# Kernel tuning notes

Hardware: AMD Instinct MI355X
Metric: run time of the kernel (lower is better)

## Reference

```python
import jax, jax.numpy as jnp
import numpy as np

N = 20000      # total atoms per branch
M = 12         # max neighbors
ORIG = 92      # orig_atom_fea_len
NBR = 41       # nbr_fea_len
F = 64         # atom_fea_len
H = 128        # h_fea_len
NCONV = 3
NH = 1
NCRYS = 400    # crystals in batch
EPS = 1e-5


def _bn_params(k, c):
    k1, k2, k3, k4 = jax.random.split(k, 4)
    g = 1.0 + 0.1 * jax.random.normal(k1, (c,), jnp.float32)
    b = 0.1 * jax.random.normal(k2, (c,), jnp.float32)
    m = 0.1 * jax.random.normal(k3, (c,), jnp.float32)
    v = 1.0 + 0.1 * jnp.abs(jax.random.normal(k4, (c,), jnp.float32))
    return jnp.stack([g, b, m, v], axis=0)  # (4, c)


def setup_inputs():
    key = jax.random.key(0)
    ks = iter(jax.random.split(key, 64))
    inp = {}
    for s in ('A', 'B'):
        inp[f'atom_fea_{s}'] = jax.random.normal(next(ks), (N, ORIG), jnp.float32)
        inp[f'nbr_fea_{s}'] = jax.random.uniform(next(ks), (N, M, NBR), jnp.float32)
        inp[f'nbr_fea_idx_{s}'] = jax.random.randint(next(ks), (N, M), 0, N)
        inp[f'crystal_atom_idx_{s}'] = jnp.sort(jax.random.randint(next(ks), (N,), 0, NCRYS))
        inp[f'emb_W_{s}'] = 0.05 * jax.random.normal(next(ks), (ORIG, F), jnp.float32)
        inp[f'emb_b_{s}'] = jnp.zeros((F,), jnp.float32)
        inp[f'conv_W_{s}'] = 0.05 * jax.random.normal(next(ks), (NCONV, 2 * F + NBR, 2 * F), jnp.float32)
        inp[f'conv_b_{s}'] = jnp.zeros((NCONV, 2 * F), jnp.float32)
        inp[f'conv_bn1_{s}'] = jnp.stack([_bn_params(next(ks), 2 * F) for _ in range(NCONV)])  # (NCONV,4,2F)
        inp[f'conv_bn2_{s}'] = jnp.stack([_bn_params(next(ks), F) for _ in range(NCONV)])      # (NCONV,4,F)
        inp[f'dense_W_{s}'] = 0.05 * jax.random.normal(next(ks), (F, H), jnp.float32)
        inp[f'dense_b_{s}'] = jnp.zeros((H,), jnp.float32)
    inp['ff_W'] = 0.05 * jax.random.normal(next(ks), (NH, H, H), jnp.float32)
    inp['ff_b'] = jnp.zeros((NH, H), jnp.float32)
    inp['out_W'] = 0.05 * jax.random.normal(next(ks), (H, 1), jnp.float32)
    inp['out_b'] = jnp.zeros((1,), jnp.float32)
    return inp


def _bn_eval(x, p):
    # eval-mode batchnorm: (x - mean) / sqrt(var + eps) * gamma + beta
    g, b, m, v = p[0], p[1], p[2], p[3]
    return (x - m) * (g * jax.lax.rsqrt(v + EPS)) + b


def _conv_layer(x, nbr_fea, nbr_idx, W, b, bn1, bn2):
    # x: (N,F); nbr_fea: (N,M,NBR); nbr_idx: (N,M)
    nbr = x[nbr_idx]                                              # gather (N,M,F)
    self_f = jnp.broadcast_to(x[:, None, :], nbr.shape)          # (N,M,F)
    tot = jnp.concatenate([self_f, nbr, nbr_fea], axis=2)        # (N,M,2F+NBR)
    z = _bn_eval(tot @ W + b, bn1)                               # (N,M,2F)
    filt, core = jnp.split(z, 2, axis=2)
    s = jnp.sum(jax.nn.sigmoid(filt) * jax.nn.softplus(core), axis=1)  # (N,F)
    s = _bn_eval(s, bn2)
    return jax.nn.softplus(x + s)


def _pool_mean(x, seg):
    s = jax.ops.segment_sum(x, seg, num_segments=NCRYS)
    cnt = jax.ops.segment_sum(jnp.ones((x.shape[0], 1), x.dtype), seg, num_segments=NCRYS)
    return s / jnp.maximum(cnt, 1.0)


def _branch(atom_fea, nbr_fea, nbr_idx, seg, emb_W, emb_b, conv_W, conv_b, bn1, bn2, dense_W, dense_b):
    a = atom_fea @ emb_W + emb_b
    for i in range(NCONV):
        a = _conv_layer(a, nbr_fea, nbr_idx, conv_W[i], conv_b[i], bn1[i], bn2[i])
    return jax.nn.softplus(_pool_mean(a, seg) @ dense_W + dense_b)  # (NCRYS,H)


def reference(atom_fea_A, nbr_fea_A, nbr_fea_idx_A, crystal_atom_idx_A,
              atom_fea_B, nbr_fea_B, nbr_fea_idx_B, crystal_atom_idx_B,
              emb_W_A, emb_b_A, conv_W_A, conv_b_A, conv_bn1_A, conv_bn2_A, dense_W_A, dense_b_A,
              emb_W_B, emb_b_B, conv_W_B, conv_b_B, conv_bn1_B, conv_bn2_B, dense_W_B, dense_b_B,
              ff_W, ff_b, out_W, out_b):
    crys_A = _branch(atom_fea_A, nbr_fea_A, nbr_fea_idx_A, crystal_atom_idx_A,
                     emb_W_A, emb_b_A, conv_W_A, conv_b_A, conv_bn1_A, conv_bn2_A, dense_W_A, dense_b_A)
    crys_B = _branch(atom_fea_B, nbr_fea_B, nbr_fea_idx_B, crystal_atom_idx_B,
                     emb_W_B, emb_b_B, conv_W_B, conv_b_B, conv_bn1_B, conv_bn2_B, dense_W_B, dense_b_B)
    crys = jnp.abs(crys_A - crys_B)  # combine_features == 'subtract_abs'
    for i in range(NH):              # dropout is identity in eval mode
        crys = jax.nn.softplus(crys @ ff_W[i] + ff_b[i])
    return crys @ out_W + out_b      # (NCRYS, 1)
```

## Files before the change

kernel.cpp:

```cpp
#include <hip/hip_runtime.h>


constexpr int NATOM = 20000;
constexpr int MNBR  = 12;
constexpr int ORIG  = 92;
constexpr int NBRF  = 41;
constexpr int F     = 64;
constexpr int H     = 128;
constexpr int NCONV = 3;
constexpr int NCRYS = 400;

#define DEVFN __device__ __forceinline__

typedef __attribute__((ext_vector_type(8))) short short8;
typedef __attribute__((ext_vector_type(4))) float f32x4;

DEVFN float softplusf(float x) {
    return fmaxf(x, 0.f) + __logf(1.f + __expf(-fabsf(x)));
}
DEVFN float sigmoidf(float x) {
    return __builtin_amdgcn_rcpf(1.f + __expf(-x));
}
DEVFN unsigned short f2bf(float x) {
    union { float f; unsigned u; } v{x};
    unsigned r = v.u + 0x7FFF + ((v.u >> 16) & 1);
    return (unsigned short)(r >> 16);
}
DEVFN float bf2f(unsigned short h) {
    union { unsigned u; float f; } v;
    v.u = (unsigned)h << 16;
    return v.f;
}
DEVFN unsigned pk2(float a, float b) {
    return (unsigned)f2bf(a) | ((unsigned)f2bf(b) << 16);
}
DEVFN unsigned short f2h(float x) {
    _Float16 h = (_Float16)x;
    union { _Float16 h; unsigned short u; } v{h};
    return v.u;
}
DEVFN float h2f(unsigned short u) {
    union { unsigned short u; _Float16 h; } v{u};
    return (float)v.h;
}
DEVFN unsigned packlo(unsigned a, unsigned b) { return (a & 0xffffu) | (b << 16); }
DEVFN unsigned packhi(unsigned a, unsigned b) { return (a >> 16) | (b & 0xffff0000u); }

__global__ __launch_bounds__(256) void k_wcvt(const float* __restrict__ convW_A,
                                              const float* __restrict__ convW_B,
                                              const float* __restrict__ embWA,
                                              const float* __restrict__ embWB,
                                              unsigned* __restrict__ w3t,
                                              unsigned* __restrict__ w12h,
                                              unsigned* __restrict__ w12l,
                                              unsigned* __restrict__ embh,
                                              unsigned* __restrict__ embl) {
    int e = blockIdx.x * 256 + threadIdx.x;
    if (e < 24576) {
        int mat = e >> 12;
        int rem = e & 4095;
        int col = rem >> 5, kp = rem & 31, k = kp * 2;
        int br = mat / 3, l = mat - br * 3;
        const float* src = (br ? convW_B : convW_A) + (size_t)l * (2 * F + NBRF) * H + 128 * H;
        float v0 = (k < NBRF) ? src[k * H + col] : 0.f;
        float v1 = (k + 1 < NBRF) ? src[(k + 1) * H + col] : 0.f;
        w3t[e] = pk2(v0, v1);
    } else if (e < 73728) {
        int e2 = e - 24576;
        int mat = e2 >> 13;
        int rem = e2 & 8191;
        int col = rem >> 5, kp = rem & 31, k = kp * 2;
        const float* src = (mat >= 3 ? convW_B : convW_A) + (size_t)(mat % 3) * (2 * F + NBRF) * H;
        float v0, v1;
        if (col < 128) { v0 = src[k * H + col];              v1 = src[(k + 1) * H + col]; }
        else           { v0 = src[(64 + k) * H + col - 128]; v1 = src[(64 + k + 1) * H + col - 128]; }
        unsigned short h0 = f2bf(v0), h1 = f2bf(v1);
        w12h[e2] = (unsigned)h0 | ((unsigned)h1 << 16);
        w12l[e2] = (unsigned)f2bf(v0 - bf2f(h0)) | ((unsigned)f2bf(v1 - bf2f(h1)) << 16);
    } else {
        int e3 = e - 73728;
        int br = e3 / 3072;
        int rem = e3 - br * 3072;
        int col = rem / 48, kp = rem - col * 48, k = kp * 2;
        const float* src = br ? embWB : embWA;
        float v0 = (k < ORIG) ? src[k * F + col] : 0.f;
        float v1 = (k + 1 < ORIG) ? src[(k + 1) * F + col] : 0.f;
        unsigned short h0 = f2bf(v0), h1 = f2bf(v1);
        embh[e3] = (unsigned)h0 | ((unsigned)h1 << 16);
        embl[e3] = (unsigned)f2bf(v0 - bf2f(h0)) | ((unsigned)f2bf(v1 - bf2f(h1)) << 16);
    }
}

__global__ __launch_bounds__(256) void k_nbrcvt(const float* __restrict__ nbrA,
                                                const float* __restrict__ nbrB,
                                                uint4* __restrict__ out) {
    int e = blockIdx.x * 256 + threadIdx.x;
    int row = e / 6, sub = e - row * 6;
    int br = row >= NATOM * MNBR;
    const float* s = (br ? nbrB : nbrA) + (size_t)(row - br * NATOM * MNBR) * NBRF;
    int k0 = sub * 8;
    float v[8];
#pragma unroll
    for (int j = 0; j < 8; ++j) v[j] = (k0 + j < NBRF) ? s[k0 + j] : 0.f;
    uint4 o;
    o.x = pk2(v[0], v[1]);
    o.y = pk2(v[2], v[3]);
    o.z = pk2(v[4], v[5]);
    o.w = pk2(v[6], v[7]);
    out[e] = o;
}

__global__ __launch_bounds__(256) void k_embed(const float* __restrict__ atomA,
                                               const float* __restrict__ atomB,
                                               const unsigned* __restrict__ embh,
                                               const unsigned* __restrict__ embl,
                                               const float* __restrict__ embbA,
                                               const float* __restrict__ embbB,
                                               unsigned* __restrict__ aP) {
    __shared__ __align__(16) unsigned short sH[32 * 104];
    __shared__ __align__(16) unsigned short sL[32 * 104];
    int t = threadIdx.x;
    int atom0 = blockIdx.x * 32;
    int br = atom0 >= NATOM;
    const float* src = (br ? atomB : atomA) + (size_t)(atom0 - br * NATOM) * ORIG;

#pragma unroll
    for (int it = 0; it < 3; ++it) {
        int idx = t + it * 256;
        if (idx < 736) {
            int row = idx / 23, sub = idx - row * 23;
            float4 v = *(const float4*)(src + (size_t)row * ORIG + sub * 4);
            int o = row * 104 + sub * 4;
            unsigned short h0 = f2bf(v.x), h1 = f2bf(v.y), h2 = f2bf(v.z), h3 = f2bf(v.w);
            *(uint2*)(sH + o) = uint2{(unsigned)h0 | ((unsigned)h1 << 16),
                                      (unsigned)h2 | ((unsigned)h3 << 16)};
            *(uint2*)(sL + o) = uint2{(unsigned)f2bf(v.x - bf2f(h0)) | ((unsigned)f2bf(v.y - bf2f(h1)) << 16),
                                      (unsigned)f2bf(v.z - bf2f(h2)) | ((unsigned)f2bf(v.w - bf2f(h3)) << 16)};
        } else if (idx < 768) {
            int row = idx - 736;
            *(uint2*)(sH + row * 104 + 92) = uint2{0, 0};
            *(uint2*)(sL + row * 104 + 92) = uint2{0, 0};
        }
    }

    int w = t >> 6, lane = t & 63;
    int lr = lane & 15, lq = lane >> 4;
    int col = w * 16 + lr;

    const unsigned short* bh_base = (const unsigned short*)embh + (size_t)br * 6144 + (size_t)col * 96;
    const unsigned short* bl_base = (const unsigned short*)embl + (size_t)br * 6144 + (size_t)col * 96;
    short8 bh[3], bl[3];
#pragma unroll
    for (int ks = 0; ks < 3; ++ks) {
        bh[ks] = *(const short8*)(bh_base + ks * 32 + lq * 8);
        bl[ks] = *(const short8*)(bl_base + ks * 32 + lq * 8);
    }
    __syncthreads();

    f32x4 acc[2];
    acc[0] = f32x4{0.f, 0.f, 0.f, 0.f};
    acc[1] = f32x4{0.f, 0.f, 0.f, 0.f};
#pragma unroll
    for (int ks = 0; ks < 3; ++ks) {
        int ko = ks * 32 + lq * 8;
        short8 ah[2], al[2];
#pragma unroll
        for (int r = 0; r < 2; ++r) {
            ah[r] = *(const short8*)(sH + (r * 16 + lr) * 104 + ko);
            al[r] = *(const short8*)(sL + (r * 16 + lr) * 104 + ko);
        }
#pragma unroll
        for (int r = 0; r < 2; ++r) {
            acc[r] = __builtin_amdgcn_mfma_f32_16x16x32_bf16(ah[r], bh[ks], acc[r], 0, 0, 0);
            acc[r] = __builtin_amdgcn_mfma_f32_16x16x32_bf16(ah[r], bl[ks], acc[r], 0, 0, 0);
            acc[r] = __builtin_amdgcn_mfma_f32_16x16x32_bf16(al[r], bh[ks], acc[r], 0, 0, 0);
        }
    }

    float bias = (br ? embbB : embbA)[col];
#pragma unroll
    for (int r = 0; r < 2; ++r)
#pragma unroll
        for (int q = 0; q < 4; ++q) {
            int atom = atom0 + r * 16 + lq * 4 + q;
            float val = acc[r][q] + bias;
            unsigned short h = f2bf(val);
            aP[(size_t)atom * F + col] = (unsigned)h | ((unsigned)f2bf(val - bf2f(h)) << 16);
        }
}

__global__ __launch_bounds__(256, 2) void k_y12(const unsigned* __restrict__ aP,
                                                const unsigned* __restrict__ w12h_base,
                                                const unsigned* __restrict__ w12l_base,
                                                int layer,
                                                unsigned short* __restrict__ y1u,
                                                unsigned short* __restrict__ y2u) {
    __shared__ __align__(16) unsigned short sH[32 * 72];
    __shared__ __align__(16) unsigned short sL[32 * 72];
    int t = threadIdx.x;
    int atom0 = blockIdx.x * 32;
    int br = atom0 >= NATOM;
    int mat = br * 3 + layer;
    const unsigned short* w12h = (const unsigned short*)(w12h_base + (size_t)mat * 8192);
    const unsigned short* w12l = (const unsigned short*)(w12l_base + (size_t)mat * 8192);
#pragma unroll
    for (int it = 0; it < 2; ++it) {
        int c = t + it * 256;
        int row = c >> 4, sub = c & 15;
        uint4 u = *(const uint4*)(aP + (size_t)(atom0 + row) * 64 + sub * 4);
        *(uint2*)(sH + row * 72 + sub * 4) = uint2{packlo(u.x, u.y), packlo(u.z, u.w)};
        *(uint2*)(sL + row * 72 + sub * 4) = uint2{packhi(u.x, u.y), packhi(u.z, u.w)};
    }
    int w = t >> 6, lane = t & 63;
    int lr = lane & 15, lq = lane >> 4;

    short8 bh[2][4], bl[2][4];
#pragma unroll
    for (int kstep = 0; kstep < 2; ++kstep)
#pragma unroll
        for (int n = 0; n < 4; ++n) {
            int col = w * 64 + n * 16 + lr;
            size_t off = (size_t)col * 64 + kstep * 32 + lq * 8;
            bh[kstep][n] = *(const short8*)(w12h + off);
            bl[kstep][n] = *(const short8*)(w12l + off);
        }
    __syncthreads();

    f32x4 acc[4][2];
#pragma unroll
    for (int n = 0; n < 4; ++n)
#pragma unroll
        for (int r = 0; r < 2; ++r) acc[n][r] = f32x4{0.f, 0.f, 0.f, 0.f};

#pragma unroll
    for (int kstep = 0; kstep < 2; ++kstep) {
        int ks = kstep * 32 + lq * 8;
        short8 ah[2], al[2];
#pragma unroll
        for (int r = 0; r < 2; ++r) {
            ah[r] = *(const short8*)(sH + (r * 16 + lr) * 72 + ks);
            al[r] = *(const short8*)(sL + (r * 16 + lr) * 72 + ks);
        }
#pragma unroll
        for (int n = 0; n < 4; ++n)
#pragma unroll
            for (int r = 0; r < 2; ++r) {
                acc[n][r] = __builtin_amdgcn_mfma_f32_16x16x32_bf16(ah[r], bh[kstep][n], acc[n][r], 0, 0, 0);
                acc[n][r] = __builtin_amdgcn_mfma_f32_16x16x32_bf16(ah[r], bl[kstep][n], acc[n][r], 0, 0, 0);
                acc[n][r] = __builtin_amdgcn_mfma_f32_16x16x32_bf16(al[r], bh[kstep][n], acc[n][r], 0, 0, 0);
            }
    }

#pragma unroll
    for (int n = 0; n < 4; ++n) {
        int c = w * 64 + n * 16 + lr;
        int cc = c & 127;
        int p = cc >> 6, cb = cc & 63;
        unsigned short* base = (c < 128) ? y1u : y2u;
        unsigned short* dst = base + cb * 2 + p;
#pragma unroll
        for (int r = 0; r < 2; ++r)
#pragma unroll
            for (int q = 0; q < 4; ++q) {
                int atom = atom0 + r * 16 + lq * 4 + q;
                dst[(size_t)atom * 128] = f2h(acc[n][r][q]);
            }
    }
}

__global__ __launch_bounds__(256, 4) void k_convfused(
        const unsigned* __restrict__ y1p,
        const unsigned* __restrict__ y2p,
        const unsigned short* __restrict__ nbrb,
        const int* __restrict__ idxA, const int* __restrict__ idxB,
        const unsigned* __restrict__ w3t, int layer,
        const float* __restrict__ biasA, const float* __restrict__ biasB,
        const float* __restrict__ bn1A,  const float* __restrict__ bn1B,
        const float* __restrict__ bn2A,  const float* __restrict__ bn2B,
        unsigned* __restrict__ aP) {
    __shared__ __align__(16) unsigned char pool[27072];
    float* sZ  = (float*)pool;
    float* sS1 = (float*)(pool + 25344);
    float* sH1 = sS1 + 128;
    float* sS2 = sH1 + 128;
    float* sH2 = sS2 + 64;
    int*   sJ  = (int*)(pool + 26880);

    int t = threadIdx.x;
    int atom0 = blockIdx.x * 4;
    int br = atom0 >= NATOM;
    int brOff = br * NATOM;
    int R0 = atom0 * MNBR;
    const float* bias = br ? biasB : biasA;
    const float* bn1  = br ? bn1B : bn1A;
    const float* bn2  = br ? bn2B : bn2A;
    const unsigned short* w3l = (const unsigned short*)(w3t + (size_t)(br * 3 + layer) * 4096);

#pragma unroll
    for (int j = 0; j < 2; ++j) {
        int c = t + j * 256;
        if (c < 288) {
            int row = c / 6, sub = c - row * 6;
            short8 v = *(const short8*)(nbrb + (size_t)(R0 + row) * 48 + sub * 8);
            *(short8*)(pool + row * 144 + sub * 16) = v;
        } else if (c < 384) {
            int z = c - 288;
            int row = z >> 1, sub = 6 + (z & 1);
            *(short8*)(pool + row * 144 + sub * 16) = short8{0, 0, 0, 0, 0, 0, 0, 0};
        }
    }
    if (t < 128) {
        float g = bn1[t], be = bn1[128 + t], mu = bn1[256 + t], va = bn1[384 + t];
        float s = g * rsqrtf(va + 1e-5f);
        sS1[t] = s;
        sH1[t] = be - mu * s + bias[t] * s;
    } else if (t < 192) {
        int u = t - 128;
        float g = bn2[u], be = bn2[64 + u], mu = bn2[128 + u], va = bn2[192 + u];
        float s = g * rsqrtf(va + 1e-5f);
        sS2[u] = s;
        sH2[u] = be - mu * s;
    }
    if (t < 48) sJ[t] = ((br ? idxB : idxA) + (size_t)(atom0 - brOff) * MNBR)[t];

    int w = t >> 6, lane = t & 63;
    int lr = lane & 15, lq = lane >> 4;
    int CB = w * 32;
    short8 bfr[2][2];
#pragma unroll
    for (int kstep = 0; kstep < 2; ++kstep)
#pragma unroll
        for (int n = 0; n < 2; ++n) {
            int col = CB + n * 16 + lr;
            int ks = kstep * 32 + lq * 8;
            bfr[kstep][n] = *(const short8*)(w3l + (size_t)col * 64 + ks);
        }
    __syncthreads();

    f32x4 acc[2][3];
#pragma unroll
    for (int n = 0; n < 2; ++n)
#pragma unroll
        for (int r = 0; r < 3; ++r) acc[n][r] = f32x4{0.f, 0.f, 0.f, 0.f};

#pragma unroll
    for (int kstep = 0; kstep < 2; ++kstep) {
        int ks = kstep * 32 + lq * 8;
        short8 af[3];
#pragma unroll
        for (int r = 0; r < 3; ++r) {
            int row = r * 16 + lr;
            af[r] = *(const short8*)(pool + (size_t)row * 144 + ks * 2);
        }
#pragma unroll
        for (int n = 0; n < 2; ++n)
#pragma unroll
            for (int r = 0; r < 3; ++r)
                acc[n][r] = __builtin_amdgcn_mfma_f32_16x16x32_bf16(af[r], bfr[kstep][n], acc[n][r], 0, 0, 0);
    }
    __syncthreads();

#pragma unroll
    for (int n = 0; n < 2; ++n)
#pragma unroll
        for (int r = 0; r < 3; ++r)
#pragma unroll
            for (int q = 0; q < 4; ++q) {
                int row = r * 16 + lq * 4 + q;
                int col = CB + n * 16 + lr;
                sZ[row * 132 + col] = acc[n][r][q];
            }
    __syncthreads();

    int al = t >> 6, f = t & 63;
    int i = atom0 + al;
    unsigned y1v = y1p[(size_t)i * 64 + f];
    float y1f = h2f((unsigned short)(y1v & 0xffff));
    float y1c = h2f((unsigned short)(y1v >> 16));
    float s1f = sS1[f], h1f = sH1[f], s1c = sS1[64 + f], h1c = sH1[64 + f];

    int js[MNBR];
#pragma unroll
    for (int m = 0; m < MNBR; ++m) js[m] = sJ[al * MNBR + m] + brOff;
    unsigned gq[MNBR];
#pragma unroll
    for (int m = 0; m < MNBR; ++m) gq[m] = y2p[(size_t)js[m] * 64 + f];

    float sacc = 0.f;
#pragma unroll
    for (int m = 0; m < MNBR; ++m) {
        int row = al * MNBR + m;
        float zf = sZ[row * 132 + f] + y1f + h2f((unsigned short)(gq[m] & 0xffff));
        float zc = sZ[row * 132 + 64 + f] + y1c + h2f((unsigned short)(gq[m] >> 16));
        zf = zf * s1f + h1f;
        zc = zc * s1c + h1c;
        sacc += sigmoidf(zf) * softplusf(zc);
    }
    size_t o = (size_t)i * 64 + f;
    unsigned au = aP[o];
    float av = bf2f((unsigned short)(au & 0xffff)) + bf2f((unsigned short)(au >> 16));
    float res = softplusf(av + sacc * sS2[f] + sH2[f]);
    unsigned short hh = f2bf(res);
    aP[o] = (unsigned)hh | ((unsigned)f2bf(res - bf2f(hh)) << 16);
}

__global__ __launch_bounds__(256) void k_pool(const unsigned* __restrict__ aP,
                                              const int* __restrict__ segA,
                                              const int* __restrict__ segB,
                                              float* __restrict__ poolU,
                                              float* __restrict__ cntU) {
    int t = threadIdx.x;
    int f = t & 63, g = t >> 6;
    int n0 = blockIdx.x * 16 + g * 4;
    int br = n0 >= NATOM;
    const int* seg = br ? segB : segA;
    int nl = n0 - br * NATOM;
    int s0 = seg[nl], s1 = seg[nl + 1], s2 = seg[nl + 2], s3 = seg[nl + 3];
    unsigned u0 = aP[(size_t)(n0 + 0) * F + f];
    unsigned u1 = aP[(size_t)(n0 + 1) * F + f];
    unsigned u2 = aP[(size_t)(n0 + 2) * F + f];
    unsigned u3 = aP[(size_t)(n0 + 3) * F + f];
    float v0 = bf2f((unsigned short)(u0 & 0xffff)) + bf2f((unsigned short)(u0 >> 16));
    float v1 = bf2f((unsigned short)(u1 & 0xffff)) + bf2f((unsigned short)(u1 >> 16));
    float v2 = bf2f((unsigned short)(u2 & 0xffff)) + bf2f((unsigned short)(u2 >> 16));
    float v3 = bf2f((unsigned short)(u3 & 0xffff)) + bf2f((unsigned short)(u3 >> 16));
    int cOff = br * NCRYS;
    if (s0 == s3) {
        atomicAdd(&poolU[(size_t)(s0 + cOff) * F + f], v0 + v1 + v2 + v3);
        if (f == 0) atomicAdd(&cntU[s0 + cOff], 4.f);
    } else {
        atomicAdd(&poolU[(size_t)(s0 + cOff) * F + f], v0);
        atomicAdd(&poolU[(size_t)(s1 + cOff) * F + f], v1);
        atomicAdd(&poolU[(size_t)(s2 + cOff) * F + f], v2);
        atomicAdd(&poolU[(size_t)(s3 + cOff) * F + f], v3);
        if (f == 0) {
            atomicAdd(&cntU[s0 + cOff], 1.f);
            atomicAdd(&cntU[s1 + cOff], 1.f);
            atomicAdd(&cntU[s2 + cOff], 1.f);
            atomicAdd(&cntU[s3 + cOff], 1.f);
        }
    }
}

__global__ __launch_bounds__(128) void k_head(const float* __restrict__ poolU,
                                              const float* __restrict__ cntU,
                                              const float* __restrict__ denWA,
                                              const float* __restrict__ denbA,
                                              const float* __restrict__ denWB,
                                              const float* __restrict__ denbB,
                                              const float* __restrict__ ffW,
                                              const float* __restrict__ ffb,
                                              const float* __restrict__ outW,
                                              const float* __restrict__ outb,
                                              float* __restrict__ out) {
    int c = blockIdx.x;
    int h = threadIdx.x;
    __shared__ float spA[F], spB[F], sd[H], st[H];
    if (h < F) spA[h] = poolU[(size_t)c * F + h] / fmaxf(cntU[c], 1.f);
    else {
        int u = h - F;
        spB[u] = poolU[(size_t)(c + NCRYS) * F + u] / fmaxf(cntU[c + NCRYS], 1.f);
    }
    __syncthreads();
    float accA = denbA[h], accB = denbB[h];
#pragma unroll
    for (int k = 0; k < F; ++k) {
        accA = fmaf(spA[k], denWA[k * H + h], accA);
        accB = fmaf(spB[k], denWB[k * H + h], accB);
    }
    sd[h] = fabsf(softplusf(accA) - softplusf(accB));
    __syncthreads();
    float acc = ffb[h];
#pragma unroll
    for (int k = 0; k < H; ++k) acc = fmaf(sd[k], ffW[k * H + h], acc);
    st[h] = softplusf(acc) * outW[h];
    __syncthreads();
    for (int s = 64; s > 0; s >>= 1) {
        if (h < s) st[h] += st[h + s];
        __syncthreads();
    }
    if (h == 0) out[c] = st[0] + outb[0];
}

extern "C" void kernel_launch(void* const* d_in, const int* in_sizes, int n_in,
                              void* d_out, int out_size, void* d_ws, size_t ws_size,
                              hipStream_t stream) {
    const float* atomA = (const float*)d_in[0];
    const float* nbrA  = (const float*)d_in[1];
    const int*   idxA  = (const int*)d_in[2];
    const int*   segA  = (const int*)d_in[3];
    const float* embWA = (const float*)d_in[4];
    const float* embbA = (const float*)d_in[5];
    const float* convWA = (const float*)d_in[6];
    const float* convbA = (const float*)d_in[7];
    const float* bn1A  = (const float*)d_in[8];
    const float* bn2A  = (const float*)d_in[9];
    const float* denWA = (const float*)d_in[10];
    const float* denbA = (const float*)d_in[11];
    const float* atomB = (const float*)d_in[12];
    const float* nbrB  = (const float*)d_in[13];
    const int*   idxB  = (const int*)d_in[14];
    const int*   segB  = (const int*)d_in[15];
    const float* embWB = (const float*)d_in[16];
    const float* embbB = (const float*)d_in[17];
    const float* convWB = (const float*)d_in[18];
    const float* convbB = (const float*)d_in[19];
    const float* bn1B  = (const float*)d_in[20];
    const float* bn2B  = (const float*)d_in[21];
    const float* denWB = (const float*)d_in[22];
    const float* denbB = (const float*)d_in[23];
    const float* ffW   = (const float*)d_in[24];
    const float* ffb   = (const float*)d_in[25];
    const float* outW  = (const float*)d_in[26];
    const float* outb  = (const float*)d_in[27];

    unsigned* y1p = (unsigned*)d_ws;
    unsigned* y2p = y1p + (size_t)2 * NATOM * 64;
    float* poolU = (float*)(y2p + (size_t)2 * NATOM * 64);
    float* cntU  = poolU + 2 * NCRYS * F;
    unsigned* w3t  = (unsigned*)(cntU + 2 * NCRYS);
    unsigned* w12h = w3t + 24576;
    unsigned* w12l = w12h + 49152;
    unsigned* embh = w12l + 49152;
    unsigned* embl = embh + 6144;
    unsigned* nbrb = embl + 6144;
    unsigned* aP   = nbrb + (size_t)2 * NATOM * MNBR * 24;

    hipMemsetAsync(poolU, 0, (size_t)(2 * NCRYS * F + 2 * NCRYS) * sizeof(float), stream);
    k_wcvt<<<312, 256, 0, stream>>>(convWA, convWB, embWA, embWB, w3t, w12h, w12l, embh, embl);
    k_nbrcvt<<<2 * NATOM * MNBR * 6 / 256, 256, 0, stream>>>(nbrA, nbrB, (uint4*)nbrb);
    k_embed<<<2 * NATOM / 32, 256, 0, stream>>>(atomA, atomB, embh, embl, embbA, embbB, aP);
    for (int l = 0; l < NCONV; ++l) {
        k_y12<<<2 * NATOM / 32, 256, 0, stream>>>(aP, w12h, w12l, l,
                                                  (unsigned short*)y1p, (unsigned short*)y2p);
        k_convfused<<<2 * NATOM / 4, 256, 0, stream>>>(
            y1p, y2p, (const unsigned short*)nbrb, idxA, idxB, w3t, l,
            convbA + l * H, convbB + l * H,
            bn1A + l * 4 * H, bn1B + l * 4 * H,
            bn2A + l * 4 * F, bn2B + l * 4 * F,
            aP);
    }
    k_pool<<<2 * NATOM * F / (256 * 4), 256, 0, stream>>>(aP, segA, segB, poolU, cntU);
    k_head<<<NCRYS, 128, 0, stream>>>(poolU, cntU, denWA, denbA, denWB, denbB,
                                      ffW, ffb, outW, outb, (float*)d_out);
}
```

Baseline: 248.0 us.

## Consume MFMA accumulators directly in gated epilogue, shrink LDS, raise occupancy

Each wave now owns matching filter and core columns (f and 64+f), so the gate epilogue runs straight from the MFMA accumulator registers. This removes the 25 KB shared-memory staging of the Z matrix and one barrier. Per-lane partial sums over groups of four neighbors go to a small LDS array and are reduced per atom afterwards. Launch bounds rise to 6 blocks per SM, relying on the smaller LDS footprint. Gather loads are now spread across lanes with fewer loads in flight per thread.

```diff
diff --git a/kernel.cpp b/kernel.cpp
--- a/kernel.cpp
+++ b/kernel.cpp
@@ -268,7 +268,7 @@
     }
 }
 
-__global__ __launch_bounds__(256, 4) void k_convfused(
+__global__ __launch_bounds__(256, 6) void k_convfused(
         const unsigned* __restrict__ y1p,
         const unsigned* __restrict__ y2p,
         const unsigned short* __restrict__ nbrb,
@@ -278,13 +278,10 @@
         const float* __restrict__ bn1A,  const float* __restrict__ bn1B,
         const float* __restrict__ bn2A,  const float* __restrict__ bn2B,
         unsigned* __restrict__ aP) {
-    __shared__ __align__(16) unsigned char pool[27072];
-    float* sZ  = (float*)pool;
-    float* sS1 = (float*)(pool + 25344);
-    float* sH1 = sS1 + 128;
-    float* sS2 = sH1 + 128;
-    float* sH2 = sS2 + 64;
-    int*   sJ  = (int*)(pool + 26880);
+    __shared__ __align__(16) unsigned char sAbuf[6912];
+    __shared__ float sS1[128], sH1[128], sS2[64], sH2[64];
+    __shared__ float sp[12 * 65 + 3];
+    __shared__ __align__(16) int sJ[48];
 
     int t = threadIdx.x;
     int atom0 = blockIdx.x * 4;
@@ -302,11 +299,11 @@
         if (c < 288) {
             int row = c / 6, sub = c - row * 6;
             short8 v = *(const short8*)(nbrb + (size_t)(R0 + row) * 48 + sub * 8);
-            *(short8*)(pool + row * 144 + sub * 16) = v;
+            *(short8*)(sAbuf + row * 144 + sub * 16) = v;
         } else if (c < 384) {
             int z = c - 288;
             int row = z >> 1, sub = 6 + (z & 1);
-            *(short8*)(pool + row * 144 + sub * 16) = short8{0, 0, 0, 0, 0, 0, 0, 0};
+            *(short8*)(sAbuf + row * 144 + sub * 16) = short8{0, 0, 0, 0, 0, 0, 0, 0};
         }
     }
     if (t < 128) {
@@ -325,16 +322,15 @@
 
     int w = t >> 6, lane = t & 63;
     int lr = lane & 15, lq = lane >> 4;
-    int CB = w * 32;
+    int f = w * 16 + lr;
+
     short8 bfr[2][2];
 #pragma unroll
-    for (int kstep = 0; kstep < 2; ++kstep)
-#pragma unroll
-        for (int n = 0; n < 2; ++n) {
-            int col = CB + n * 16 + lr;
-            int ks = kstep * 32 + lq * 8;
-            bfr[kstep][n] = *(const short8*)(w3l + (size_t)col * 64 + ks);
-        }
+    for (int kstep = 0; kstep < 2; ++kstep) {
+        int ks = kstep * 32 + lq * 8;
+        bfr[kstep][0] = *(const short8*)(w3l + (size_t)f * 64 + ks);
+        bfr[kstep][1] = *(const short8*)(w3l + (size_t)(64 + f) * 64 + ks);
+    }
     __syncthreads();
 
     f32x4 acc[2][3];
@@ -350,7 +346,7 @@
 #pragma unroll
         for (int r = 0; r < 3; ++r) {
             int row = r * 16 + lr;
-            af[r] = *(const short8*)(pool + (size_t)row * 144 + ks * 2);
+            af[r] = *(const short8*)(sAbuf + (size_t)row * 144 + ks * 2);
         }
 #pragma unroll
         for (int n = 0; n < 2; ++n)
@@ -358,48 +354,38 @@
             for (int r = 0; r < 3; ++r)
                 acc[n][r] = __builtin_amdgcn_mfma_f32_16x16x32_bf16(af[r], bfr[kstep][n], acc[n][r], 0, 0, 0);
     }
-    __syncthreads();
-
-#pragma unroll
-    for (int n = 0; n < 2; ++n)
-#pragma unroll
-        for (int r = 0; r < 3; ++r)
-#pragma unroll
-            for (int q = 0; q < 4; ++q) {
-                int row = r * 16 + lq * 4 + q;
-                int col = CB + n * 16 + lr;
-                sZ[row * 132 + col] = acc[n][r][q];
-            }
-    __syncthreads();
-
-    int al = t >> 6, f = t & 63;
-    int i = atom0 + al;
-    unsigned y1v = y1p[(size_t)i * 64 + f];
-    float y1f = h2f((unsigned short)(y1v & 0xffff));
-    float y1c = h2f((unsigned short)(y1v >> 16));
+
     float s1f = sS1[f], h1f = sH1[f], s1c = sS1[64 + f], h1c = sH1[64 + f];
-
-    int js[MNBR];
-#pragma unroll
-    for (int m = 0; m < MNBR; ++m) js[m] = sJ[al * MNBR + m] + brOff;
-    unsigned gq[MNBR];
-#pragma unroll
-    for (int m = 0; m < MNBR; ++m) gq[m] = y2p[(size_t)js[m] * 64 + f];
-
-    float sacc = 0.f;
-#pragma unroll
-    for (int m = 0; m < MNBR; ++m) {
-        int row = al * MNBR + m;
-        float zf = sZ[row * 132 + f] + y1f + h2f((unsigned short)(gq[m] & 0xffff));
-        float zc = sZ[row * 132 + 64 + f] + y1c + h2f((unsigned short)(gq[m] >> 16));
-        zf = zf * s1f + h1f;
-        zc = zc * s1c + h1c;
-        sacc += sigmoidf(zf) * softplusf(zc);
-    }
-    size_t o = (size_t)i * 64 + f;
+#pragma unroll
+    for (int r = 0; r < 3; ++r) {
+        int rowbase = 16 * r + 4 * lq;
+        int4 jq = *(const int4*)(sJ + rowbase);
+        int atom = (4 * r + lq) / 3;
+        unsigned y1v = y1p[(size_t)(atom0 + atom) * 64 + f];
+        float y1f = h2f((unsigned short)(y1v & 0xffff));
+        float y1c = h2f((unsigned short)(y1v >> 16));
+        float partial = 0.f;
+        unsigned g0 = y2p[(size_t)(jq.x + brOff) * 64 + f];
+        unsigned g1 = y2p[(size_t)(jq.y + brOff) * 64 + f];
+        unsigned g2 = y2p[(size_t)(jq.z + brOff) * 64 + f];
+        unsigned g3 = y2p[(size_t)(jq.w + brOff) * 64 + f];
+        unsigned gv[4] = {g0, g1, g2, g3};
+#pragma unroll
+        for (int q = 0; q < 4; ++q) {
+            float zf = (acc[0][r][q] + y1f + h2f((unsigned short)(gv[q] & 0xffff))) * s1f + h1f;
+            float zc = (acc[1][r][q] + y1c + h2f((unsigned short)(gv[q] >> 16))) * s1c + h1c;
+            partial += sigmoidf(zf) * softplusf(zc);
+        }
+        sp[(4 * r + lq) * 65 + f] = partial;
+    }
+    __syncthreads();
+
+    int al = t >> 6, f2 = t & 63;
+    float sacc = sp[(3 * al + 0) * 65 + f2] + sp[(3 * al + 1) * 65 + f2] + sp[(3 * al + 2) * 65 + f2];
+    size_t o = (size_t)(atom0 + al) * 64 + f2;
     unsigned au = aP[o];
     float av = bf2f((unsigned short)(au & 0xffff)) + bf2f((unsigned short)(au >> 16));
-    float res = softplusf(av + sacc * sS2[f] + sH2[f]);
+    float res = softplusf(av + sacc * sS2[f2] + sH2[f2]);
     unsigned short hh = f2bf(res);
     aP[o] = (unsigned)hh | ((unsigned)f2bf(res - bf2f(hh)) << 16);
 }
```

Result: no change. 250.1 us (+0.8%).
